# Optimization experiments

Hardware: AMD Instinct MI355X
Metric: run time of the kernel (lower is better)

Reference implementation:

```python
import jax, jax.numpy as jnp
import numpy as np

B, S, D, H, HD = 2, 2048, 1024, 16, 64
LN_EPS = 1e-6


def setup_inputs() -> dict:
    key = jax.random.key(0)
    ks = jax.random.split(key, 4)
    x = jax.random.normal(ks[0], (B, S, D), dtype=jnp.float32)
    ln_scale = jnp.ones((D,), jnp.float32)
    ln_bias = jnp.zeros((D,), jnp.float32)
    w_qkv = jax.random.normal(ks[1], (D, H, 3 * HD), jnp.float32) * (D ** -0.5)
    b_qkv = jnp.zeros((H, 3 * HD), jnp.float32)
    w_out = jax.random.normal(ks[2], (H, HD, D), jnp.float32) * ((H * HD) ** -0.5)
    b_out = jnp.zeros((D,), jnp.float32)
    # causal mask, broadcastable to weights shape [B, H, q, k]
    mask = jnp.tril(jnp.ones((S, S), dtype=bool))[None, None, :, :]
    return {"x": x, "ln_scale": ln_scale, "ln_bias": ln_bias,
            "w_qkv": w_qkv, "b_qkv": b_qkv, "w_out": w_out, "b_out": b_out,
            "mask": mask}


def _attention_block(x, ln_scale, ln_bias, w_qkv, b_qkv, w_out, b_out, mask):
    # Pre-LayerNorm
    mu = jnp.mean(x, axis=-1, keepdims=True)
    var = jnp.mean(jnp.square(x - mu), axis=-1, keepdims=True)
    xn = (x - mu) * jax.lax.rsqrt(var + LN_EPS) * ln_scale + ln_bias
    # QKV projection: [B,S,D] x [D,H,3*hd] -> [B,S,H,3*hd]
    qkv = jnp.einsum('bsd,dhf->bshf', xn, w_qkv) + b_qkv
    q, k, v = jnp.split(qkv, 3, axis=-1)  # each [B,S,H,hd]
    # scaled dot-product attention in float32 (softmax_dtype)
    scale = HD ** -0.5
    qf = (q * scale).astype(jnp.float32)
    kf = k.astype(jnp.float32)
    weights = jnp.einsum('bqhd,bkhd->bhqk', qf, kf)  # [B,H,S,S]
    weights = jnp.where(mask, weights, jnp.finfo(jnp.float32).min)
    weights = jax.nn.softmax(weights, axis=-1).astype(x.dtype)
    attn = jnp.einsum('bhqk,bkhd->bqhd', weights, v)  # [B,S,H,hd]
    # output projection, contracting (H, hd)
    out = jnp.einsum('bqhd,hdf->bqf', attn, w_out) + b_out  # [B,S,D]
    return out


def reference(x, ln_scale, ln_bias, w_qkv, b_qkv, w_out, b_out, mask):
    return _attention_block(x, ln_scale, ln_bias, w_qkv, b_qkv, w_out, b_out, mask)
```

## Files before the change

### kernel.cpp

```cpp
#include <hip/hip_runtime.h>
#include <hip/hip_bf16.h>
#include <stdint.h>

#define B_ 2
#define S_ 2048
#define D_ 1024
#define H_ 16
#define HD_ 64
#define M_ (B_*S_)
#define NQKV_ (H_*3*HD_)

typedef __attribute__((ext_vector_type(8))) short short8;
typedef __attribute__((ext_vector_type(4))) float f32x4;
typedef unsigned short u16;
typedef unsigned int u32;

__device__ __forceinline__ u16 f2b(float f){
  u32 u = __float_as_uint(f);
  u32 r = (u + 0x7FFFu + ((u >> 16) & 1u)) >> 16;
  return (u16)r;
}

__device__ __forceinline__ float exp2v(float x){
  float r; asm("v_exp_f32 %0, %1" : "=v"(r) : "v"(x)); return r;
}

__device__ __forceinline__ void gl_lds16(const void* g, void* l){
  __builtin_amdgcn_global_load_lds(
      (const __attribute__((address_space(1))) void*)g,
      (__attribute__((address_space(3))) void*)l, 16, 0, 0);
}

__global__ __launch_bounds__(256) void ln_kernel(const float* __restrict__ x,
    const float* __restrict__ gam, const float* __restrict__ bet, u16* __restrict__ xn){
  int row = blockIdx.x;
  const float4* xr = (const float4*)(x + (size_t)row * D_);
  float4 v = xr[threadIdx.x];
  float s = v.x + v.y + v.z + v.w;
  float q = v.x*v.x + v.y*v.y + v.z*v.z + v.w*v.w;
  #pragma unroll
  for(int o = 32; o > 0; o >>= 1){ s += __shfl_down(s, o); q += __shfl_down(q, o); }
  __shared__ float red[8];
  int w = threadIdx.x >> 6, lane = threadIdx.x & 63;
  if(lane == 0){ red[w] = s; red[4+w] = q; }
  __syncthreads();
  float st = red[0]+red[1]+red[2]+red[3];
  float qt = red[4]+red[5]+red[6]+red[7];
  float mu = st * (1.0f / D_);
  float inv = rsqrtf(qt * (1.0f / D_) - mu*mu + 1e-6f);
  float4 g = ((const float4*)gam)[threadIdx.x];
  float4 b = ((const float4*)bet)[threadIdx.x];
  ushort4 o4;
  o4.x = f2b((v.x-mu)*inv*g.x + b.x);
  o4.y = f2b((v.y-mu)*inv*g.y + b.y);
  o4.z = f2b((v.z-mu)*inv*g.z + b.z);
  o4.w = f2b((v.w-mu)*inv*g.w + b.w);
  ((ushort4*)(xn + (size_t)row * D_))[threadIdx.x] = o4;
}

__global__ __launch_bounds__(256) void tconv_kernel(const float* __restrict__ src,
    u16* __restrict__ dst, int R, int C){
  __shared__ float tile[64][65];
  int tx = threadIdx.x & 63, ty = threadIdx.x >> 6;
  int r0 = blockIdx.y * 64, c0 = blockIdx.x * 64;
  #pragma unroll
  for(int i = 0; i < 16; i++){
    int r = ty*16 + i;
    tile[r][tx] = src[(size_t)(r0+r)*C + c0 + tx];
  }
  __syncthreads();
  #pragma unroll
  for(int i = 0; i < 16; i++){
    int r = ty*16 + i;
    dst[(size_t)(c0+r)*R + r0 + tx] = f2b(tile[tx][r]);
  }
}

__global__ __launch_bounds__(256) void vtrans_kernel(const u16* __restrict__ V, u16* __restrict__ Vt){
  __shared__ u16 t2[64][66];
  int tx = threadIdx.x & 63, ty = threadIdx.x >> 6;
  int bh = blockIdx.y, s0 = blockIdx.x * 64;
  const u16* src = V + (size_t)bh * S_ * HD_;
  u16* dst = Vt + (size_t)bh * HD_ * S_;
  #pragma unroll
  for(int i = 0; i < 16; i++){
    int r = ty*16 + i;
    t2[r][tx] = src[(size_t)(s0+r)*HD_ + tx];
  }
  __syncthreads();
  #pragma unroll
  for(int i = 0; i < 16; i++){
    int hd = ty*16 + i;
    dst[(size_t)hd*S_ + s0 + tx] = t2[tx][hd];
  }
}

__global__ __launch_bounds__(512, 1) void gemm256_kernel(const u16* __restrict__ A,
    const u16* __restrict__ Bt, const float* __restrict__ bias,
    u16* __restrict__ o0, u16* __restrict__ o1, u16* __restrict__ o2){
  constexpr int K_ = 1024;
  __shared__ __align__(16) char smem[114688];
  int tid = threadIdx.x, w = tid >> 6, lane = tid & 63;
  int wm = w >> 1, wn = w & 1;
  int bid = blockIdx.y * gridDim.x + blockIdx.x;
  int nwg = gridDim.x * gridDim.y;
  int cpx = nwg >> 3;
  int swz = (bid & 7) * cpx + (bid >> 3);
  int m0 = (swz / gridDim.x) * 256, n0 = (swz % gridDim.x) * 192;

  f32x4 z = {0.f, 0.f, 0.f, 0.f};
  f32x4 acc[4][6];
  #pragma unroll
  for(int r = 0; r < 4; r++)
    #pragma unroll
    for(int c = 0; c < 6; c++) acc[r][c] = z;

  int srow8 = tid >> 3;
  int sch = (tid & 7) ^ (srow8 & 7);
  auto STAGE_A = [&](int buf, int half, int kt){
    #pragma unroll
    for(int l = 0; l < 2; l++){
      int row = half*128 + l*64 + srow8;
      gl_lds16(A + (size_t)(m0 + row)*K_ + kt*64 + sch*8,
               smem + buf*32768 + half*16384 + l*8192 + tid*16);
    }
  };
  auto STAGE_B3 = [&](int slot, int third, int kt){
    int row = third*64 + srow8;
    gl_lds16(Bt + (size_t)(n0 + row)*K_ + kt*64 + sch*8,
             smem + 65536 + slot*24576 + third*8192 + tid*16);
  };

  int ln15 = lane & 15, g = lane >> 4;
  int co0 = ((g    ) ^ (ln15 & 7)) * 16;
  int co1 = ((4 + g) ^ (ln15 & 7)) * 16;
  auto LDA = [&](int buf, int r, int k)->short8{
    int row = wm*64 + r*16 + ln15;
    return *(const short8*)(smem + buf*32768 + row*128 + (k ? co1 : co0));
  };
  auto LDB = [&](int slot, int c, int k)->short8{
    int row = wn*96 + c*16 + ln15;
    return *(const short8*)(smem + 65536 + slot*24576 + row*128 + (k ? co1 : co0));
  };
  #define BAR()   __builtin_amdgcn_s_barrier()
  #define LGKM0() do{ asm volatile("s_waitcnt lgkmcnt(0)" ::: "memory"); \
                      __builtin_amdgcn_sched_barrier(0); }while(0)
  #define MF(r_, c_, a_, b_) acc[r_][c_] = __builtin_amdgcn_mfma_f32_16x16x32_bf16(a_, b_, acc[r_][c_], 0, 0, 0)

  constexpr int nk = K_ / 64;
  STAGE_A(0, 0, 0); STAGE_A(0, 1, 0);
  STAGE_B3(0, 0, 0); STAGE_B3(0, 1, 0); STAGE_B3(0, 2, 0);
  STAGE_B3(1, 0, 1); STAGE_B3(1, 1, 1); STAGE_B3(1, 2, 1);
  asm volatile("s_waitcnt vmcnt(3)" ::: "memory");
  __builtin_amdgcn_sched_barrier(0);
  BAR();

  #pragma unroll 2
  for(int t = 0; t < nk; t++){
    int buf = t & 1;
    int kA = (t + 1 < nk) ? t + 1 : nk - 1;
    int kB = (t + 2 < nk) ? t + 2 : nk - 1;
    short8 a[4][2], b01[2][2], b23[2][2], b45[2][2];
    #pragma unroll
    for(int r = 0; r < 4; r++){ a[r][0] = LDA(buf, r, 0); a[r][1] = LDA(buf, r, 1); }
    #pragma unroll
    for(int c = 0; c < 2; c++){ b01[c][0] = LDB(buf, c, 0); b01[c][1] = LDB(buf, c, 1); }
    STAGE_A(buf ^ 1, 0, kA);
    BAR(); LGKM0();
    __builtin_amdgcn_s_setprio(1);
    #pragma unroll
    for(int r = 0; r < 4; r++)
      #pragma unroll
      for(int c = 0; c < 2; c++){ MF(r, c, a[r][0], b01[c][0]); MF(r, c, a[r][1], b01[c][1]); }
    __builtin_amdgcn_s_setprio(0);
    BAR();
    #pragma unroll
    for(int c = 0; c < 2; c++){ b23[c][0] = LDB(buf, c + 2, 0); b23[c][1] = LDB(buf, c + 2, 1); }
    STAGE_A(buf ^ 1, 1, kA);
    BAR(); LGKM0();
    __builtin_amdgcn_s_setprio(1);
    #pragma unroll
    for(int r = 0; r < 4; r++)
      #pragma unroll
      for(int c = 0; c < 2; c++){ MF(r, c+2, a[r][0], b23[c][0]); MF(r, c+2, a[r][1], b23[c][1]); }
    __builtin_amdgcn_s_setprio(0);
    BAR();
    #pragma unroll
    for(int c = 0; c < 2; c++){ b45[c][0] = LDB(buf, c + 4, 0); b45[c][1] = LDB(buf, c + 4, 1); }
    BAR(); LGKM0();
    __builtin_amdgcn_s_setprio(1);
    #pragma unroll
    for(int r = 0; r < 4; r++){ MF(r, 4, a[r][0], b45[0][0]); MF(r, 4, a[r][1], b45[0][1]); }
    __builtin_amdgcn_s_setprio(0);
    BAR();
    STAGE_B3(buf, 0, kB); STAGE_B3(buf, 1, kB); STAGE_B3(buf, 2, kB);
    BAR();
    __builtin_amdgcn_s_setprio(1);
    #pragma unroll
    for(int r = 0; r < 4; r++){ MF(r, 5, a[r][0], b45[1][0]); MF(r, 5, a[r][1], b45[1][1]); }
    __builtin_amdgcn_s_setprio(0);
    asm volatile("s_waitcnt vmcnt(3)" ::: "memory");
    __builtin_amdgcn_sched_barrier(0);
    BAR();
  }
  #undef BAR
  #undef LGKM0
  #undef MF

  #pragma unroll
  for(int r = 0; r < 4; r++){
    #pragma unroll
    for(int c = 0; c < 6; c++){
      #pragma unroll
      for(int q = 0; q < 4; q++){
        int row = m0 + wm*64 + r*16 + g*4 + q;
        int col = n0 + wn*96 + c*16 + ln15;
        float v = acc[r][c][q] + bias[col];
        int h = col / 192, rr = col - h*192;
        int b = row >> 11, s = row & (S_ - 1);
        size_t base = ((size_t)(b*H_ + h)*S_ + s) * HD_;
        if(rr < 64)        o0[base + rr]       = f2b(v * 0.180336884f);
        else if(rr < 128)  o1[base + rr - 64]  = f2b(v);
        else               o2[base + rr - 128] = f2b(v);
      }
    }
  }
}

__global__ __launch_bounds__(256) void gemm_kernel(const u16* __restrict__ A,
    const u16* __restrict__ Bt, const float* __restrict__ bias,
    float* __restrict__ out, int K, int N){
  __shared__ u16 As[2][128*32];
  __shared__ u16 Bs[2][128*32];
  int tid = threadIdx.x, w = tid >> 6, lane = tid & 63;
  int bid = blockIdx.y * gridDim.x + blockIdx.x;
  int nwg = gridDim.x * gridDim.y;
  int cpx = nwg >> 3;
  int swz = (bid & 7) * cpx + (bid >> 3);
  int m0 = (swz / gridDim.x) * 128, n0 = (swz % gridDim.x) * 128;
  int wm = w >> 1, wn = w & 1;
  f32x4 z = {0.f, 0.f, 0.f, 0.f};
  f32x4 acc[4][4];
  #pragma unroll
  for(int r = 0; r < 4; r++)
    #pragma unroll
    for(int c = 0; c < 4; c++) acc[r][c] = z;
  int srow = lane >> 2, sch = (lane & 3) * 8;
  const u16* Ag = A + (size_t)m0 * K + (size_t)srow * K + sch;
  const u16* Bg = Bt + (size_t)n0 * K + (size_t)srow * K + sch;

  auto STAGE = [&](int buf, int kt){
    #pragma unroll
    for(int i = 0; i < 2; i++){
      int rb = w*32 + i*16;
      gl_lds16(Ag + (size_t)rb*K + kt, &As[buf][rb*32]);
      gl_lds16(Bg + (size_t)rb*K + kt, &Bs[buf][rb*32]);
    }
  };

  int nk = K >> 5;
  STAGE(0, 0);
  asm volatile("s_waitcnt vmcnt(0)" ::: "memory");
  __builtin_amdgcn_sched_barrier(0);
  __builtin_amdgcn_s_barrier();
  for(int t = 0; t < nk; t++){
    int cur = t & 1;
    if(t + 1 < nk){
      STAGE(cur ^ 1, (t + 1) * 32);
      asm volatile("s_waitcnt vmcnt(4)" ::: "memory");
    } else {
      asm volatile("s_waitcnt vmcnt(0)" ::: "memory");
    }
    __builtin_amdgcn_sched_barrier(0);
    __builtin_amdgcn_s_barrier();
    int kc = (lane >> 4) * 8;
    int ar = wm*64 + (lane & 15);
    int bc = wn*64 + (lane & 15);
    short8 af[4], bfr[4];
    #pragma unroll
    for(int r = 0; r < 4; r++) af[r] = *(const short8*)&As[cur][(ar + r*16)*32 + kc];
    #pragma unroll
    for(int c = 0; c < 4; c++) bfr[c] = *(const short8*)&Bs[cur][(bc + c*16)*32 + kc];
    __builtin_amdgcn_s_setprio(1);
    #pragma unroll
    for(int r = 0; r < 4; r++)
      #pragma unroll
      for(int c = 0; c < 4; c++)
        acc[r][c] = __builtin_amdgcn_mfma_f32_16x16x32_bf16(af[r], bfr[c], acc[r][c], 0, 0, 0);
    __builtin_amdgcn_s_setprio(0);
    asm volatile("" ::: "memory");
    __builtin_amdgcn_s_barrier();
  }

  #pragma unroll
  for(int r = 0; r < 4; r++){
    #pragma unroll
    for(int c = 0; c < 4; c++){
      #pragma unroll
      for(int q = 0; q < 4; q++){
        int row = m0 + wm*64 + r*16 + (lane >> 4)*4 + q;
        int col = n0 + wn*64 + c*16 + (lane & 15);
        out[(size_t)row * N + col] = acc[r][c][q] + bias[col];
      }
    }
  }
}


template<int HALF>
__device__ __forceinline__ void compute_tile(
    const char* KsB, const char* VsB, char* Pw, const short8* qf,
    f32x4* o, float& m_run, float& l_run, bool diag, int lane, int wr){
  constexpr int KB0 = (HALF == 1) ? 2 : 0;
  constexpr int KBN = (HALF == -1) ? 4 : 2;
  f32x4 z = {0.f, 0.f, 0.f, 0.f};
  f32x4 sf[4];
  __builtin_amdgcn_s_setprio(1);
  #pragma unroll
  for(int kb = KB0; kb < KB0 + KBN; kb++){
    f32x4 acc = z;
    #pragma unroll
    for(int c = 0; c < 2; c++){
      int row = kb*16 + (lane & 15);
      int kc16 = (lane >> 4) + c*4;
      short8 kf = *(const short8*)(KsB + row*128 + ((kc16 ^ (row & 7)) * 16));
      acc = __builtin_amdgcn_mfma_f32_16x16x32_bf16(kf, qf[c], acc, 0, 0, 0);
    }
    sf[kb] = acc;
  }
  __builtin_amdgcn_s_setprio(0);
  if(diag){
    int qo = wr*16 + (lane & 15);
    #pragma unroll
    for(int kb = KB0; kb < KB0 + KBN; kb++)
      #pragma unroll
      for(int r = 0; r < 4; r++){
        int kvo = kb*16 + (lane >> 4)*4 + r;
        if(kvo > qo) sf[kb][r] = -1e30f;
      }
  }
  int g = lane >> 4;
  float pmax = -1e28f;
  #pragma unroll
  for(int kb = KB0; kb < KB0 + KBN; kb++)
    pmax = fmaxf(pmax, fmaxf(fmaxf(sf[kb][0], sf[kb][1]), fmaxf(sf[kb][2], sf[kb][3])));
  pmax = fmaxf(pmax, __shfl_xor(pmax, 16));
  pmax = fmaxf(pmax, __shfl_xor(pmax, 32));
  if(!__all(pmax <= m_run + 8.f)){
    float mn = fmaxf(m_run, pmax);
    float al = exp2v(m_run - mn);
    m_run = mn;
    l_run *= al;
    float alr[4];
    #pragma unroll
    for(int r = 0; r < 4; r++) alr[r] = __shfl(al, g*4 + r);
    #pragma unroll
    for(int n = 0; n < 4; n++)
      #pragma unroll
      for(int r = 0; r < 4; r++) o[n][r] *= alr[r];
  }
  float p[4][4];
  float sum = 0.f;
  #pragma unroll
  for(int kb = KB0; kb < KB0 + KBN; kb++){
    #pragma unroll
    for(int r = 0; r < 4; r++) p[kb][r] = exp2v(sf[kb][r] - m_run);
    sum += (p[kb][0]+p[kb][1]) + (p[kb][2]+p[kb][3]);
  }
  sum += __shfl_xor(sum, 16);
  sum += __shfl_xor(sum, 32);
  l_run += sum;
  int qrow = lane & 15;
  #pragma unroll
  for(int kb = KB0; kb < KB0 + KBN; kb++){
    u32 lo, hi;
    asm("v_cvt_pk_bf16_f32 %0, %1, %2" : "=v"(lo) : "v"(p[kb][0]), "v"(p[kb][1]));
    asm("v_cvt_pk_bf16_f32 %0, %1, %2" : "=v"(hi) : "v"(p[kb][2]), "v"(p[kb][3]));
    uint2 pk; pk.x = lo; pk.y = hi;
    int byt = (qrow*128 + kb*32 + g*8) ^ ((qrow & 7) << 4);
    *(uint2*)(Pw + byt) = pk;
  }
  constexpr int C0 = (HALF == 1) ? 1 : 0;
  constexpr int C1 = (HALF == 0) ? 0 : 1;
  __builtin_amdgcn_s_setprio(1);
  #pragma unroll
  for(int c = C0; c <= C1; c++){
    int prow = lane & 15;
    int kb16 = ((lane >> 4) + c*4) * 16;
    short8 pa = *(const short8*)(Pw + ((prow*128 + kb16) ^ ((prow & 7) << 4)));
    #pragma unroll
    for(int n = 0; n < 4; n++){
      int vrow = n*16 + (lane & 15);
      int kc16 = (lane >> 4) + c*4;
      short8 vf = *(const short8*)(VsB + vrow*128 + ((kc16 ^ (vrow & 7)) * 16));
      o[n] = __builtin_amdgcn_mfma_f32_16x16x32_bf16(pa, vf, o[n], 0, 0, 0);
    }
  }
  __builtin_amdgcn_s_setprio(0);
}

__global__ __launch_bounds__(512) void attn_kernel(const u16* __restrict__ Q,
    const u16* __restrict__ Kb, const u16* __restrict__ Vt, u16* __restrict__ O){
  __shared__ __align__(16) char smem[49152];
  char* PsBase = smem + 32768;
  int tid = threadIdx.x, w = tid >> 6, lane = tid & 63;
  int wr = w & 3, role = w >> 2;
  int L = blockIdx.x;
  int pi = (L >> 3) & 15;
  int bh = (L & 7) + 8 * (L >> 7);
  const int NT = S_ / 64;
  int ta = pi, tb = NT - 1 - pi;
  const u16* Qg = Q + (size_t)bh * S_ * HD_;
  const u16* Kg = Kb + (size_t)bh * S_ * HD_;
  const u16* Vg = Vt + (size_t)bh * HD_ * S_;
  int b = bh >> 4, h = bh & 15;

  short8 qb[2], qa[2];
  {
    int rb_ = tb*64 + wr*16 + (lane & 15);
    #pragma unroll
    for(int c = 0; c < 2; c++)
      qb[c] = *(const short8*)(Qg + (size_t)rb_*HD_ + (lane >> 4)*8 + c*32);
    if(role == 1){
      int ra_ = ta*64 + wr*16 + (lane & 15);
      #pragma unroll
      for(int c = 0; c < 2; c++)
        qa[c] = *(const short8*)(Qg + (size_t)ra_*HD_ + (lane >> 4)*8 + c*32);
    }
  }
  f32x4 z = {0.f, 0.f, 0.f, 0.f};
  f32x4 o[4];
  float m_run = -1e30f, l_run = 0.f;
  #pragma unroll
  for(int i = 0; i < 4; i++) o[i] = z;
  int svrow = lane >> 3, scb = lane & 7;

  auto STAGE = [&](int buf, int kt){
    int kv0 = kt * 64;
    int rowblk = w * 8;
    int row = rowblk + svrow;
    int cbs = scb ^ (row & 7);
    gl_lds16(Kg + (size_t)(kv0 + row)*HD_ + cbs*8, smem + buf*8192 + rowblk*128);
    gl_lds16(Vg + (size_t)row*S_ + kv0 + cbs*8, smem + 16384 + buf*8192 + rowblk*128);
  };

  STAGE(0, 0);
  asm volatile("s_waitcnt vmcnt(0)" ::: "memory");
  __builtin_amdgcn_sched_barrier(0);
  __builtin_amdgcn_s_barrier();
  int cur = 0;
  char* Pw = PsBase + w*2048;
  for(int kt = 0; kt <= tb; kt++){
    if(kt < tb){
      STAGE(cur ^ 1, kt + 1);
      asm volatile("s_waitcnt vmcnt(2)" ::: "memory");
    } else {
      asm volatile("s_waitcnt vmcnt(0)" ::: "memory");
    }
    __builtin_amdgcn_sched_barrier(0);
    __builtin_amdgcn_s_barrier();
    const char* KsB = (const char*)(smem + cur*8192);
    const char* VsB = (const char*)(smem + 16384 + cur*8192);
    if(role == 0){
      if(kt <= ta) compute_tile<-1>(KsB, VsB, Pw, qb, o, m_run, l_run, false, lane, wr);
      else         compute_tile<0>(KsB, VsB, Pw, qb, o, m_run, l_run, kt == tb, lane, wr);
    } else {
      if(kt <= ta){
        compute_tile<-1>(KsB, VsB, Pw, qa, o, m_run, l_run, kt == ta, lane, wr);
        if(kt == ta){
          float linv = 1.f / l_run;
          float invr[4];
          #pragma unroll
          for(int r = 0; r < 4; r++) invr[r] = __shfl(linv, (lane >> 4)*4 + r);
          #pragma unroll
          for(int n = 0; n < 4; n++)
            #pragma unroll
            for(int r = 0; r < 4; r++){
              int s = ta*64 + wr*16 + (lane >> 4)*4 + r;
              int hd = n*16 + (lane & 15);
              O[(((size_t)(b*S_ + s))*H_ + h)*HD_ + hd] = f2b(o[n][r] * invr[r]);
            }
          m_run = -1e30f; l_run = 0.f;
          #pragma unroll
          for(int i = 0; i < 4; i++) o[i] = z;
        }
      } else {
        compute_tile<1>(KsB, VsB, Pw, qb, o, m_run, l_run, kt == tb, lane, wr);
      }
    }
    asm volatile("" ::: "memory");
    __builtin_amdgcn_s_barrier();
    cur ^= 1;
  }

  float* Mg = (float*)smem + wr*1072;
  if(role == 1){
    #pragma unroll
    for(int n = 0; n < 4; n++)
      #pragma unroll
      for(int r = 0; r < 4; r++)
        Mg[((lane >> 4)*4 + r)*65 + n*16 + (lane & 15)] = o[n][r];
    if(lane < 16){ Mg[1040 + lane] = m_run; Mg[1056 + lane] = l_run; }
  }
  __syncthreads();
  if(role == 0){
    float F1[4], F2[4], den[4];
    #pragma unroll
    for(int r = 0; r < 4; r++){
      int row = (lane >> 4)*4 + r;
      float m1r = __shfl(m_run, row);
      float l1r = __shfl(l_run, row);
      float m2r = Mg[1040 + row];
      float l2r = Mg[1056 + row];
      float mm = fmaxf(m1r, m2r);
      F1[r] = exp2v(m1r - mm);
      F2[r] = exp2v(m2r - mm);
      den[r] = 1.f / (l1r*F1[r] + l2r*F2[r]);
    }
    #pragma unroll
    for(int n = 0; n < 4; n++)
      #pragma unroll
      for(int r = 0; r < 4; r++){
        int row = (lane >> 4)*4 + r;
        float o2 = Mg[row*65 + n*16 + (lane & 15)];
        float val = (o[n][r]*F1[r] + o2*F2[r]) * den[r];
        int s = tb*64 + wr*16 + row;
        int hd = n*16 + (lane & 15);
        O[(((size_t)(b*S_ + s))*H_ + h)*HD_ + hd] = f2b(val);
      }
  }
}

extern "C" void kernel_launch(void* const* d_in, const int* in_sizes, int n_in,
                              void* d_out, int out_size, void* d_ws, size_t ws_size,
                              hipStream_t stream){
  (void)in_sizes; (void)n_in; (void)out_size; (void)ws_size;
  const float* x    = (const float*)d_in[0];
  const float* gam  = (const float*)d_in[1];
  const float* bet  = (const float*)d_in[2];
  const float* wqkv = (const float*)d_in[3];
  const float* bqkv = (const float*)d_in[4];
  const float* wout = (const float*)d_in[5];
  const float* bout = (const float*)d_in[6];
  char* ws = (char*)d_ws;
  u16* xn    = (u16*)(ws);
  u16* wqkvT = (u16*)(ws + 8388608);
  u16* woutT = (u16*)(ws + 8388608 + 6291456);
  u16* Qb    = (u16*)(ws + 16777216);
  u16* Kb    = (u16*)(ws + 16777216 + 8388608);
  u16* Vb    = (u16*)(ws + 16777216 + 2*8388608);
  u16* Vt    = (u16*)(ws + 16777216 + 3*8388608);
  u16* attnb = xn;
  float* out = (float*)d_out;

  ln_kernel<<<dim3(M_), dim3(256), 0, stream>>>(x, gam, bet, xn);
  tconv_kernel<<<dim3(NQKV_/64, D_/64), dim3(256), 0, stream>>>(wqkv, wqkvT, D_, NQKV_);
  tconv_kernel<<<dim3(D_/64, D_/64), dim3(256), 0, stream>>>(wout, woutT, D_, D_);
  gemm256_kernel<<<dim3(NQKV_/192, M_/256), dim3(512), 0, stream>>>(xn, wqkvT, bqkv, Qb, Kb, Vb);
  vtrans_kernel<<<dim3(S_/64, B_*H_), dim3(256), 0, stream>>>(Vb, Vt);
  attn_kernel<<<dim3(512), dim3(512), 0, stream>>>(Qb, Kb, Vt, attnb);
  gemm_kernel<<<dim3(D_/128, M_/128), dim3(256), 0, stream>>>(attnb, woutT, bout, out, D_, D_);
}
```

Measured before the change: 123.0 us.

## Read K/V fragments directly from global memory instead of staging through LDS

Removes the double-buffered global-to-LDS staging of K and V tiles along with the per-iteration block barriers. Each wave now loads its MFMA K and V fragments straight from global memory and relies on L1/L2 for reuse. Shared memory drops to the per-wave P buffers plus the merge area, and a min-blocks launch bound is added to raise occupancy. The trade-off is redundant global and cache traffic across the 8 waves, plus exposed load latency with no explicit prefetch.

```diff
diff --git a/kernel.cpp b/kernel.cpp
--- a/kernel.cpp
+++ b/kernel.cpp
@@ -309,11 +309,12 @@
 
 template<int HALF>
 __device__ __forceinline__ void compute_tile(
-    const char* KsB, const char* VsB, char* Pw, const short8* qf,
-    f32x4* o, float& m_run, float& l_run, bool diag, int lane, int wr){
+    const u16* __restrict__ Kg, const u16* __restrict__ Vg, int kv0, char* Pw,
+    const short8* qf, f32x4* o, float& m_run, float& l_run, bool diag, int lane, int wr){
   constexpr int KB0 = (HALF == 1) ? 2 : 0;
   constexpr int KBN = (HALF == -1) ? 4 : 2;
   f32x4 z = {0.f, 0.f, 0.f, 0.f};
+  int ln15 = lane & 15, g = lane >> 4;
   f32x4 sf[4];
   __builtin_amdgcn_s_setprio(1);
   #pragma unroll
@@ -321,25 +322,22 @@
     f32x4 acc = z;
     #pragma unroll
     for(int c = 0; c < 2; c++){
-      int row = kb*16 + (lane & 15);
-      int kc16 = (lane >> 4) + c*4;
-      short8 kf = *(const short8*)(KsB + row*128 + ((kc16 ^ (row & 7)) * 16));
+      short8 kf = *(const short8*)(Kg + (size_t)(kv0 + kb*16 + ln15)*HD_ + (g + c*4)*8);
       acc = __builtin_amdgcn_mfma_f32_16x16x32_bf16(kf, qf[c], acc, 0, 0, 0);
     }
     sf[kb] = acc;
   }
   __builtin_amdgcn_s_setprio(0);
   if(diag){
-    int qo = wr*16 + (lane & 15);
+    int qo = wr*16 + ln15;
     #pragma unroll
     for(int kb = KB0; kb < KB0 + KBN; kb++)
       #pragma unroll
       for(int r = 0; r < 4; r++){
-        int kvo = kb*16 + (lane >> 4)*4 + r;
+        int kvo = kb*16 + g*4 + r;
         if(kvo > qo) sf[kb][r] = -1e30f;
       }
   }
-  int g = lane >> 4;
   float pmax = -1e28f;
   #pragma unroll
   for(int kb = KB0; kb < KB0 + KBN; kb++)
@@ -370,14 +368,13 @@
   sum += __shfl_xor(sum, 16);
   sum += __shfl_xor(sum, 32);
   l_run += sum;
-  int qrow = lane & 15;
   #pragma unroll
   for(int kb = KB0; kb < KB0 + KBN; kb++){
     u32 lo, hi;
     asm("v_cvt_pk_bf16_f32 %0, %1, %2" : "=v"(lo) : "v"(p[kb][0]), "v"(p[kb][1]));
     asm("v_cvt_pk_bf16_f32 %0, %1, %2" : "=v"(hi) : "v"(p[kb][2]), "v"(p[kb][3]));
     uint2 pk; pk.x = lo; pk.y = hi;
-    int byt = (qrow*128 + kb*32 + g*8) ^ ((qrow & 7) << 4);
+    int byt = (ln15*128 + kb*32 + g*8) ^ ((ln15 & 7) << 4);
     *(uint2*)(Pw + byt) = pk;
   }
   constexpr int C0 = (HALF == 1) ? 1 : 0;
@@ -385,24 +382,20 @@
   __builtin_amdgcn_s_setprio(1);
   #pragma unroll
   for(int c = C0; c <= C1; c++){
-    int prow = lane & 15;
-    int kb16 = ((lane >> 4) + c*4) * 16;
-    short8 pa = *(const short8*)(Pw + ((prow*128 + kb16) ^ ((prow & 7) << 4)));
+    int kb16 = (g + c*4) * 16;
+    short8 pa = *(const short8*)(Pw + ((ln15*128 + kb16) ^ ((ln15 & 7) << 4)));
     #pragma unroll
     for(int n = 0; n < 4; n++){
-      int vrow = n*16 + (lane & 15);
-      int kc16 = (lane >> 4) + c*4;
-      short8 vf = *(const short8*)(VsB + vrow*128 + ((kc16 ^ (vrow & 7)) * 16));
+      short8 vf = *(const short8*)(Vg + (size_t)(n*16 + ln15)*S_ + kv0 + (g + c*4)*8);
       o[n] = __builtin_amdgcn_mfma_f32_16x16x32_bf16(pa, vf, o[n], 0, 0, 0);
     }
   }
   __builtin_amdgcn_s_setprio(0);
 }
 
-__global__ __launch_bounds__(512) void attn_kernel(const u16* __restrict__ Q,
+__global__ __launch_bounds__(512, 4) void attn_kernel(const u16* __restrict__ Q,
     const u16* __restrict__ Kb, const u16* __restrict__ Vt, u16* __restrict__ O){
-  __shared__ __align__(16) char smem[49152];
-  char* PsBase = smem + 32768;
+  __shared__ __align__(16) char smem[33792];
   int tid = threadIdx.x, w = tid >> 6, lane = tid & 63;
   int wr = w & 3, role = w >> 2;
   int L = blockIdx.x;
@@ -433,40 +426,16 @@
   float m_run = -1e30f, l_run = 0.f;
   #pragma unroll
   for(int i = 0; i < 4; i++) o[i] = z;
-  int svrow = lane >> 3, scb = lane & 7;
-
-  auto STAGE = [&](int buf, int kt){
+  char* Pw = smem + w*2048;
+
+  for(int kt = 0; kt <= tb; kt++){
     int kv0 = kt * 64;
-    int rowblk = w * 8;
-    int row = rowblk + svrow;
-    int cbs = scb ^ (row & 7);
-    gl_lds16(Kg + (size_t)(kv0 + row)*HD_ + cbs*8, smem + buf*8192 + rowblk*128);
-    gl_lds16(Vg + (size_t)row*S_ + kv0 + cbs*8, smem + 16384 + buf*8192 + rowblk*128);
-  };
-
-  STAGE(0, 0);
-  asm volatile("s_waitcnt vmcnt(0)" ::: "memory");
-  __builtin_amdgcn_sched_barrier(0);
-  __builtin_amdgcn_s_barrier();
-  int cur = 0;
-  char* Pw = PsBase + w*2048;
-  for(int kt = 0; kt <= tb; kt++){
-    if(kt < tb){
-      STAGE(cur ^ 1, kt + 1);
-      asm volatile("s_waitcnt vmcnt(2)" ::: "memory");
-    } else {
-      asm volatile("s_waitcnt vmcnt(0)" ::: "memory");
-    }
-    __builtin_amdgcn_sched_barrier(0);
-    __builtin_amdgcn_s_barrier();
-    const char* KsB = (const char*)(smem + cur*8192);
-    const char* VsB = (const char*)(smem + 16384 + cur*8192);
     if(role == 0){
-      if(kt <= ta) compute_tile<-1>(KsB, VsB, Pw, qb, o, m_run, l_run, false, lane, wr);
-      else         compute_tile<0>(KsB, VsB, Pw, qb, o, m_run, l_run, kt == tb, lane, wr);
+      if(kt <= ta) compute_tile<-1>(Kg, Vg, kv0, Pw, qb, o, m_run, l_run, false, lane, wr);
+      else         compute_tile<0>(Kg, Vg, kv0, Pw, qb, o, m_run, l_run, kt == tb, lane, wr);
     } else {
       if(kt <= ta){
-        compute_tile<-1>(KsB, VsB, Pw, qa, o, m_run, l_run, kt == ta, lane, wr);
+        compute_tile<-1>(Kg, Vg, kv0, Pw, qa, o, m_run, l_run, kt == ta, lane, wr);
         if(kt == ta){
           float linv = 1.f / l_run;
           float invr[4];
@@ -485,15 +454,12 @@
           for(int i = 0; i < 4; i++) o[i] = z;
         }
       } else {
-        compute_tile<1>(KsB, VsB, Pw, qb, o, m_run, l_run, kt == tb, lane, wr);
+        compute_tile<1>(Kg, Vg, kv0, Pw, qb, o, m_run, l_run, kt == tb, lane, wr);
       }
     }
-    asm volatile("" ::: "memory");
-    __builtin_amdgcn_s_barrier();
-    cur ^= 1;
-  }
-
-  float* Mg = (float*)smem + wr*1072;
+  }
+
+  float* Mg = (float*)(smem + 16384) + wr*1072;
   if(role == 1){
     #pragma unroll
     for(int n = 0; n < 4; n++)
```

New measurement: 200.1 us. 62.7% more time.

## Merge LN and weight transposes into one launch; write V transposed from QKV GEMM

Applied to the files above, without the earlier changes.

Combines the layernorm and both weight transpose-convert kernels into a single prep kernel that dispatches on block index, removing two launches. The QKV GEMM epilogue now writes V directly in the transposed [hd, S] layout, which removes the separate V transpose kernel and its extra read and write of V. The transposed store is strided along S, so the epilogue writes for V become less coalesced.

```diff
diff --git a/kernel.cpp b/kernel.cpp
--- a/kernel.cpp
+++ b/kernel.cpp
@@ -31,38 +31,52 @@
       (__attribute__((address_space(3))) void*)l, 16, 0, 0);
 }
 
-__global__ __launch_bounds__(256) void ln_kernel(const float* __restrict__ x,
-    const float* __restrict__ gam, const float* __restrict__ bet, u16* __restrict__ xn){
-  int row = blockIdx.x;
-  const float4* xr = (const float4*)(x + (size_t)row * D_);
-  float4 v = xr[threadIdx.x];
-  float s = v.x + v.y + v.z + v.w;
-  float q = v.x*v.x + v.y*v.y + v.z*v.z + v.w*v.w;
-  #pragma unroll
-  for(int o = 32; o > 0; o >>= 1){ s += __shfl_down(s, o); q += __shfl_down(q, o); }
-  __shared__ float red[8];
-  int w = threadIdx.x >> 6, lane = threadIdx.x & 63;
-  if(lane == 0){ red[w] = s; red[4+w] = q; }
-  __syncthreads();
-  float st = red[0]+red[1]+red[2]+red[3];
-  float qt = red[4]+red[5]+red[6]+red[7];
-  float mu = st * (1.0f / D_);
-  float inv = rsqrtf(qt * (1.0f / D_) - mu*mu + 1e-6f);
-  float4 g = ((const float4*)gam)[threadIdx.x];
-  float4 b = ((const float4*)bet)[threadIdx.x];
-  ushort4 o4;
-  o4.x = f2b((v.x-mu)*inv*g.x + b.x);
-  o4.y = f2b((v.y-mu)*inv*g.y + b.y);
-  o4.z = f2b((v.z-mu)*inv*g.z + b.z);
-  o4.w = f2b((v.w-mu)*inv*g.w + b.w);
-  ((ushort4*)(xn + (size_t)row * D_))[threadIdx.x] = o4;
-}
-
-__global__ __launch_bounds__(256) void tconv_kernel(const float* __restrict__ src,
-    u16* __restrict__ dst, int R, int C){
+__global__ __launch_bounds__(256) void prep_kernel(
+    const float* __restrict__ x, const float* __restrict__ gam,
+    const float* __restrict__ bet, u16* __restrict__ xn,
+    const float* __restrict__ wqkv, u16* __restrict__ wqkvT,
+    const float* __restrict__ wout, u16* __restrict__ woutT){
+  int bid = blockIdx.x;
   __shared__ float tile[64][65];
+  if(bid < M_){
+    int row = bid;
+    const float4* xr = (const float4*)(x + (size_t)row * D_);
+    float4 v = xr[threadIdx.x];
+    float s = v.x + v.y + v.z + v.w;
+    float q = v.x*v.x + v.y*v.y + v.z*v.z + v.w*v.w;
+    #pragma unroll
+    for(int o = 32; o > 0; o >>= 1){ s += __shfl_down(s, o); q += __shfl_down(q, o); }
+    float* red = &tile[0][0];
+    int w = threadIdx.x >> 6, lane = threadIdx.x & 63;
+    if(lane == 0){ red[w] = s; red[4+w] = q; }
+    __syncthreads();
+    float st = red[0]+red[1]+red[2]+red[3];
+    float qt = red[4]+red[5]+red[6]+red[7];
+    float mu = st * (1.0f / D_);
+    float inv = rsqrtf(qt * (1.0f / D_) - mu*mu + 1e-6f);
+    float4 g = ((const float4*)gam)[threadIdx.x];
+    float4 b = ((const float4*)bet)[threadIdx.x];
+    ushort4 o4;
+    o4.x = f2b((v.x-mu)*inv*g.x + b.x);
+    o4.y = f2b((v.y-mu)*inv*g.y + b.y);
+    o4.z = f2b((v.z-mu)*inv*g.z + b.z);
+    o4.w = f2b((v.w-mu)*inv*g.w + b.w);
+    ((ushort4*)(xn + (size_t)row * D_))[threadIdx.x] = o4;
+    return;
+  }
+  const float* src; u16* dst; int C, cx, ry;
+  if(bid < M_ + (NQKV_/64)*(D_/64)){
+    int idx = bid - M_;
+    cx = idx % (NQKV_/64); ry = idx / (NQKV_/64);
+    src = wqkv; dst = wqkvT; C = NQKV_;
+  } else {
+    int idx = bid - M_ - (NQKV_/64)*(D_/64);
+    cx = idx % (D_/64); ry = idx / (D_/64);
+    src = wout; dst = woutT; C = D_;
+  }
+  const int R = D_;
   int tx = threadIdx.x & 63, ty = threadIdx.x >> 6;
-  int r0 = blockIdx.y * 64, c0 = blockIdx.x * 64;
+  int r0 = ry * 64, c0 = cx * 64;
   #pragma unroll
   for(int i = 0; i < 16; i++){
     int r = ty*16 + i;
@@ -76,28 +90,9 @@
   }
 }
 
-__global__ __launch_bounds__(256) void vtrans_kernel(const u16* __restrict__ V, u16* __restrict__ Vt){
-  __shared__ u16 t2[64][66];
-  int tx = threadIdx.x & 63, ty = threadIdx.x >> 6;
-  int bh = blockIdx.y, s0 = blockIdx.x * 64;
-  const u16* src = V + (size_t)bh * S_ * HD_;
-  u16* dst = Vt + (size_t)bh * HD_ * S_;
-  #pragma unroll
-  for(int i = 0; i < 16; i++){
-    int r = ty*16 + i;
-    t2[r][tx] = src[(size_t)(s0+r)*HD_ + tx];
-  }
-  __syncthreads();
-  #pragma unroll
-  for(int i = 0; i < 16; i++){
-    int hd = ty*16 + i;
-    dst[(size_t)hd*S_ + s0 + tx] = t2[tx][hd];
-  }
-}
-
 __global__ __launch_bounds__(512, 1) void gemm256_kernel(const u16* __restrict__ A,
     const u16* __restrict__ Bt, const float* __restrict__ bias,
-    u16* __restrict__ o0, u16* __restrict__ o1, u16* __restrict__ o2){
+    u16* __restrict__ o0, u16* __restrict__ o1, u16* __restrict__ o2t){
   constexpr int K_ = 1024;
   __shared__ __align__(16) char smem[114688];
   int tid = threadIdx.x, w = tid >> 6, lane = tid & 63;
@@ -207,6 +202,7 @@
   #undef LGKM0
   #undef MF
 
+  int h = n0 / 192;
   #pragma unroll
   for(int r = 0; r < 4; r++){
     #pragma unroll
@@ -214,14 +210,16 @@
       #pragma unroll
       for(int q = 0; q < 4; q++){
         int row = m0 + wm*64 + r*16 + g*4 + q;
-        int col = n0 + wn*96 + c*16 + ln15;
-        float v = acc[r][c][q] + bias[col];
-        int h = col / 192, rr = col - h*192;
+        int rr = wn*96 + c*16 + ln15;
+        float v = acc[r][c][q] + bias[h*192 + rr];
         int b = row >> 11, s = row & (S_ - 1);
-        size_t base = ((size_t)(b*H_ + h)*S_ + s) * HD_;
-        if(rr < 64)        o0[base + rr]       = f2b(v * 0.180336884f);
-        else if(rr < 128)  o1[base + rr - 64]  = f2b(v);
-        else               o2[base + rr - 128] = f2b(v);
+        if(rr < 64){
+          o0[((size_t)(b*H_ + h)*S_ + s)*HD_ + rr] = f2b(v * 0.180336884f);
+        } else if(rr < 128){
+          o1[((size_t)(b*H_ + h)*S_ + s)*HD_ + rr - 64] = f2b(v);
+        } else {
+          o2t[((size_t)(b*H_ + h)*HD_ + rr - 128)*S_ + s] = f2b(v);
+        }
       }
     }
   }
@@ -548,16 +546,13 @@
   u16* woutT = (u16*)(ws + 8388608 + 6291456);
   u16* Qb    = (u16*)(ws + 16777216);
   u16* Kb    = (u16*)(ws + 16777216 + 8388608);
-  u16* Vb    = (u16*)(ws + 16777216 + 2*8388608);
-  u16* Vt    = (u16*)(ws + 16777216 + 3*8388608);
+  u16* Vt    = (u16*)(ws + 16777216 + 2*8388608);
   u16* attnb = xn;
   float* out = (float*)d_out;
 
-  ln_kernel<<<dim3(M_), dim3(256), 0, stream>>>(x, gam, bet, xn);
-  tconv_kernel<<<dim3(NQKV_/64, D_/64), dim3(256), 0, stream>>>(wqkv, wqkvT, D_, NQKV_);
-  tconv_kernel<<<dim3(D_/64, D_/64), dim3(256), 0, stream>>>(wout, woutT, D_, D_);
-  gemm256_kernel<<<dim3(NQKV_/192, M_/256), dim3(512), 0, stream>>>(xn, wqkvT, bqkv, Qb, Kb, Vb);
-  vtrans_kernel<<<dim3(S_/64, B_*H_), dim3(256), 0, stream>>>(Vb, Vt);
+  prep_kernel<<<dim3(M_ + (NQKV_/64)*(D_/64) + (D_/64)*(D_/64)), dim3(256), 0, stream>>>(
+      x, gam, bet, xn, wqkv, wqkvT, wout, woutT);
+  gemm256_kernel<<<dim3(NQKV_/192, M_/256), dim3(512), 0, stream>>>(xn, wqkvT, bqkv, Qb, Kb, Vt);
   attn_kernel<<<dim3(512), dim3(512), 0, stream>>>(Qb, Kb, Vt, attnb);
   gemm_kernel<<<dim3(D_/128, M_/128), dim3(256), 0, stream>>>(attnb, woutT, bout, out, D_, D_);
 }
```

After: 115.3 us. -6.2%, faster.
